# Performance work log

Measured on AMD Instinct MI355X. Metric: run time of the kernel, lower is better.

## Reference

```python
import jax, jax.numpy as jnp
import numpy as np

B, T, I, H = 64, 512, 512, 1024

def setup_inputs() -> dict:
    key = jax.random.key(0)
    ks = jax.random.split(key, 12)
    s_i = 1.0 / np.sqrt(I)
    s_h = 1.0 / np.sqrt(H)
    inp = {
        'x': jax.random.normal(ks[0], (B, T, I), dtype=jnp.float32),
        'h0': jnp.zeros((B, H), dtype=jnp.float32),
        'Wz': jax.random.uniform(ks[1], (H, I), jnp.float32, -s_i, s_i),
        'bz': jax.random.uniform(ks[2], (H,), jnp.float32, -s_i, s_i),
        'Uz': jax.random.uniform(ks[3], (H, H), jnp.float32, -s_h, s_h),
        'Wr': jax.random.uniform(ks[4], (H, I), jnp.float32, -s_i, s_i),
        'br': jax.random.uniform(ks[5], (H,), jnp.float32, -s_i, s_i),
        'Ur': jax.random.uniform(ks[6], (H, H), jnp.float32, -s_h, s_h),
        'Wh': jax.random.uniform(ks[7], (H, I), jnp.float32, -s_i, s_i),
        'bh': jax.random.uniform(ks[8], (H,), jnp.float32, -s_i, s_i),
        'Uh': jax.random.uniform(ks[9], (H, H), jnp.float32, -s_h, s_h),
    }
    return inp

def reference(x, h0, Wz, bz, Uz, Wr, br, Ur, Wh, bh, Uh):
    # Precompute all input projections for every timestep in 3 big GEMMs
    xz = jnp.einsum('bti,hi->bth', x, Wz) + bz  # [B,T,H]
    xr = jnp.einsum('bti,hi->bth', x, Wr) + br
    xh = jnp.einsum('bti,hi->bth', x, Wh) + bh
    # scan over time (recurrence)
    xs = (jnp.swapaxes(xz, 0, 1), jnp.swapaxes(xr, 0, 1), jnp.swapaxes(xh, 0, 1))  # [T,B,H]

    def step(h, inp):
        xz_t, xr_t, xh_t = inp
        z = jax.nn.sigmoid(xz_t + h @ Uz.T)
        r = jax.nn.sigmoid(xr_t + h @ Ur.T)
        h_tilde = jnp.tanh(xh_t + (r * h) @ Uh.T)
        h_new = (1.0 - z) * h + z * h_tilde
        return h_new, h_new

    h_last, outs = jax.lax.scan(step, h0, xs)  # outs: [T,B,H]
    outputs = jnp.swapaxes(outs, 0, 1)  # [B,T,H]
    return outputs, h_last
```

## Files before the change

kernel.cpp:

```cpp
#include <hip/hip_runtime.h>
#include <hip/hip_bf16.h>
#include <stdint.h>


#define B_ 64
#define T_ 512
#define I_ 512
#define H_ 1024
#define NWG_A 128
#define NWG_B 64
#define NWG 192
#define FSTR 64

typedef __attribute__((ext_vector_type(4))) float f32x4;
typedef __attribute__((ext_vector_type(8))) short s16x8;

__device__ __forceinline__ unsigned short f2bf(float f) {
  union { float f; uint32_t u; } v; v.f = f;
  uint32_t u = v.u;
  u += 0x7fffu + ((u >> 16) & 1u);
  return (unsigned short)(u >> 16);
}
__device__ __forceinline__ float bf2f(unsigned short h) {
  union { uint32_t u; float f; } v; v.u = ((uint32_t)h) << 16;
  return v.f;
}

__device__ __forceinline__ void sc_store_f32(float* p, float v) {
  asm volatile("global_store_dword %0, %1, off sc0 sc1"
               :: "v"(p), "v"(v) : "memory");
}
__device__ __forceinline__ void sc_store_u16(uint16_t* p, unsigned v) {
  asm volatile("global_store_short %0, %1, off sc0 sc1"
               :: "v"(p), "v"(v) : "memory");
}
__device__ __forceinline__ void sc_store_u32(unsigned* p, unsigned v) {
  asm volatile("global_store_dword %0, %1, off sc0 sc1"
               :: "v"(p), "v"(v) : "memory");
}
__device__ __forceinline__ s16x8 sc0_load_b128(const uint16_t* p) {
  s16x8 r;
  asm volatile("global_load_dwordx4 %0, %1, off sc0"
               : "=v"(r) : "v"(p) : "memory");
  return r;
}
__device__ __forceinline__ float sc0_load_f32(const float* p) {
  float r;
  asm volatile("global_load_dword %0, %1, off sc0"
               : "=v"(r) : "v"(p) : "memory");
  return r;
}
__device__ __forceinline__ void vm_drain() {
  asm volatile("s_waitcnt vmcnt(0)" ::: "memory");
}

__global__ void k_split(const float* __restrict__ src, uint16_t* __restrict__ dst,
                        int kshift, int total) {
  int K = 1 << kshift;
  for (int i = blockIdx.x * blockDim.x + threadIdx.x; i < total;
       i += gridDim.x * blockDim.x) {
    int n = i >> kshift, k = i & (K - 1);
    float f = src[i];
    unsigned short hi = f2bf(f);
    unsigned short lo = f2bf(f - bf2f(hi));
    size_t base = (size_t)n * (3 * K);
    dst[base + k] = hi;
    dst[base + K + k] = lo;
    dst[base + 2 * K + k] = hi;
  }
}

__global__ void k_init(const float* __restrict__ h0, float* __restrict__ h,
                       uint16_t* __restrict__ h2) {
  for (int i = blockIdx.x * blockDim.x + threadIdx.x; i < B_ * H_;
       i += gridDim.x * blockDim.x) {
    float f = h0[i];
    h[i] = f;
    int b = i >> 10, j = i & 1023;
    unsigned short hi = f2bf(f);
    h2[b * 2048 + j] = hi;
    h2[b * 2048 + 1024 + j] = f2bf(f - bf2f(hi));
  }
}

__global__ __launch_bounds__(256) void k_proj(
    const float* __restrict__ x, const uint16_t* __restrict__ W2,
    const float* __restrict__ bz, const float* __restrict__ br,
    const float* __restrict__ bh,
    float* __restrict__ XP, int t0, int Tc, int MT) {
  __shared__ uint16_t As[128][72];
  __shared__ uint16_t Bs[128][72];
  int bid = blockIdx.x;
  int mt = bid % MT, nt = bid / MT;
  int tid = threadIdx.x;
  int w = tid >> 6, l = tid & 63;
  int wm = w >> 1, wn = w & 1;
  int lr = l & 15, lg = l >> 4;

  int gr[4], gc8[4];
  const float* asrc[4];
  const uint16_t* bsrc[4];
#pragma unroll
  for (int g = 0; g < 4; ++g) {
    int gran = tid + 256 * g;
    int r = gran >> 3, c8 = gran & 7;
    gr[g] = r; gc8[g] = c8;
    int n = mt * 128 + r;
    int b = n / Tc, tt = n % Tc;
    asrc[g] = x + ((size_t)b * T_ + (t0 + tt)) * I_;
    bsrc[g] = W2 + (size_t)(nt * 128 + r) * 1536;
  }

  f32x4 acc[4][4];
#pragma unroll
  for (int mi = 0; mi < 4; ++mi)
#pragma unroll
    for (int ni = 0; ni < 4; ++ni) {
      acc[mi][ni][0] = 0.f; acc[mi][ni][1] = 0.f;
      acc[mi][ni][2] = 0.f; acc[mi][ni][3] = 0.f;
    }

  float4 pa[8];
  uint4 pb[4];
#pragma unroll
  for (int g = 0; g < 4; ++g) {
    int kp = gc8[g] * 8;
    int xc = kp & 511;
    pa[2 * g] = *(const float4*)(asrc[g] + xc);
    pa[2 * g + 1] = *(const float4*)(asrc[g] + xc + 4);
    pb[g] = *(const uint4*)(bsrc[g] + kp);
  }

  for (int it = 0; it < 24; ++it) {
    __syncthreads();
    {
      int k0 = it * 64;
#pragma unroll
      for (int g = 0; g < 4; ++g) {
        int kp = k0 + gc8[g] * 8;
        bool lofl = (kp >= 1024);
        const float* pf = (const float*)&pa[2 * g];
        s16x8 v;
#pragma unroll
        for (int j = 0; j < 8; ++j) {
          float f = pf[j];
          unsigned short hi = f2bf(f);
          v[j] = (short)(lofl ? f2bf(f - bf2f(hi)) : hi);
        }
        *(s16x8*)(&As[gr[g]][gc8[g] * 8]) = v;
        *(uint4*)(&Bs[gr[g]][gc8[g] * 8]) = pb[g];
      }
    }
    if (it + 1 < 24) {
      int k0 = (it + 1) * 64;
#pragma unroll
      for (int g = 0; g < 4; ++g) {
        int kp = k0 + gc8[g] * 8;
        int xc = kp & 511;
        pa[2 * g] = *(const float4*)(asrc[g] + xc);
        pa[2 * g + 1] = *(const float4*)(asrc[g] + xc + 4);
        pb[g] = *(const uint4*)(bsrc[g] + kp);
      }
    }
    __syncthreads();
#pragma unroll
    for (int kk = 0; kk < 64; kk += 32) {
      s16x8 af[4], bf[4];
#pragma unroll
      for (int mi = 0; mi < 4; ++mi)
        af[mi] = *(const s16x8*)(&As[wm * 64 + mi * 16 + lr][kk + lg * 8]);
#pragma unroll
      for (int ni = 0; ni < 4; ++ni)
        bf[ni] = *(const s16x8*)(&Bs[wn * 64 + ni * 16 + lr][kk + lg * 8]);
#pragma unroll
      for (int mi = 0; mi < 4; ++mi)
#pragma unroll
        for (int ni = 0; ni < 4; ++ni)
          acc[mi][ni] = __builtin_amdgcn_mfma_f32_16x16x32_bf16(
              af[mi], bf[ni], acc[mi][ni], 0, 0, 0);
    }
  }

  int g_ = (nt * 128) >> 10;
  const float* bias = (g_ == 0) ? bz : ((g_ == 1) ? br : bh);
#pragma unroll
  for (int ni = 0; ni < 4; ++ni) {
    int col = nt * 128 + wn * 64 + ni * 16 + lr;
    int jc = col & 1023;
    float bv = bias[jc];
#pragma unroll
    for (int mi = 0; mi < 4; ++mi) {
      int nrow = mt * 128 + wm * 64 + mi * 16 + lg * 4;
      int b = nrow / Tc, tt = nrow % Tc;
#pragma unroll
      for (int v = 0; v < 4; ++v) {
        XP[((size_t)((tt * 3 + g_) * 64 + b)) * 1024 + jc] = acc[mi][ni][v] + bv;
        if (++tt == Tc) { tt = 0; ++b; }
      }
    }
  }
}

__global__ __launch_bounds__(512) void k_recur(
    const float* __restrict__ Uz, const float* __restrict__ Ur,
    const float* __restrict__ Uh, const float* __restrict__ XP,
    int t0i, int Tcc, float* __restrict__ h, uint16_t* __restrict__ h2,
    uint16_t* __restrict__ s2, float* __restrict__ zbuf,
    float* __restrict__ out, unsigned* __restrict__ flagsA,
    unsigned* __restrict__ flagsB) {
  __shared__ uint16_t Wl[16 * 2048];
  __shared__ float red[8 * 64 * 17];

  const int tid = threadIdx.x;
  const int w = tid >> 6, l = tid & 63;
  const int lr = l & 15, lg = l >> 4;
  const int bid = blockIdx.x;
  const bool isA = (bid < NWG_A);
  const int tile = isA ? bid : (bid - NWG_A);
  const int n0 = tile * 16;
  const bool isR = isA && (n0 >= 1024);

  const float* src = isA ? ((n0 < 1024) ? (Uz + (size_t)n0 * 1024)
                                        : (Ur + (size_t)(n0 - 1024) * 1024))
                         : (Uh + (size_t)n0 * 1024);
  for (int i = tid; i < 2048; i += 512) {
    int r = i >> 7;
    int k8 = (i & 127) * 8;
    const float* p = src + r * 1024 + k8;
    s16x8 hi8, lo8;
#pragma unroll
    for (int j = 0; j < 8; ++j) {
      float f = p[j];
      unsigned short hb = f2bf(f);
      hi8[j] = (short)hb;
      lo8[j] = (short)f2bf(f - bf2f(hb));
    }
    uint8_t* rowp = (uint8_t*)Wl + r * 4096;
    int swz = (r & 7) << 4;
    *(s16x8*)(rowp + ((k8 * 2) ^ swz)) = hi8;
    *(s16x8*)(rowp + (((1024 + k8) * 2) ^ swz)) = lo8;
  }
  __syncthreads();

  const int KB0 = w * 128;
  const int bswz = (lr & 7) << 4;
  const uint8_t* browp = (const uint8_t*)Wl + lr * 4096;

  int eb[2], ec[2];
#pragma unroll
  for (int u = 0; u < 2; ++u) {
    int e = tid + u * 512;
    eb[u] = e >> 4; ec[u] = e & 15;
  }

  float hreg[2];
  if (!isA) {
#pragma unroll
    for (int u = 0; u < 2; ++u)
      hreg[u] = h[eb[u] * 1024 + (n0 + ec[u])];
  }

  for (int tt = 0; tt < Tcc; ++tt) {
    const unsigned t = (unsigned)(t0i + tt);

    float xpre[2];
    {
      int gate = isA ? (isR ? 1 : 0) : 2;
#pragma unroll
      for (int u = 0; u < 2; ++u) {
        int jc = (n0 + ec[u]) & 1023;
        xpre[u] = XP[((size_t)(tt * 3 + gate) * 64 + eb[u]) * 1024 + jc];
      }
    }

    if (isA) {
      if (t > 0 && w == 0) {
        const unsigned* fp = flagsB + (size_t)l * FSTR;
        for (;;) {
          unsigned f;
          asm volatile("global_load_dword %0, %1, off sc0 sc1\n\t"
                       "s_waitcnt vmcnt(0)"
                       : "=v"(f) : "v"(fp) : "memory");
          if (__all(f >= t)) break;
          __builtin_amdgcn_s_sleep(4);
        }
        if (l == 0)
          (void)__hip_atomic_load(flagsB, __ATOMIC_ACQUIRE,
                                  __HIP_MEMORY_SCOPE_AGENT);
        vm_drain();
      }
      __syncthreads();

      float hpre[2];
      if (isR) {
#pragma unroll
        for (int u = 0; u < 2; ++u)
          hpre[u] = sc0_load_f32(h + eb[u] * 1024 + (n0 - 1024 + ec[u]));
      }

      s16x8 ah[4][4], al[4][4];
#pragma unroll
      for (int ks = 0; ks < 4; ++ks)
#pragma unroll
        for (int mi = 0; mi < 4; ++mi)
          ah[ks][mi] = sc0_load_b128(h2 + (size_t)(lr + 16 * mi) * 2048 +
                                     (KB0 + ks * 32 + lg * 8));
#pragma unroll
      for (int ks = 0; ks < 4; ++ks)
#pragma unroll
        for (int mi = 0; mi < 4; ++mi)
          al[ks][mi] = sc0_load_b128(h2 + (size_t)(lr + 16 * mi) * 2048 +
                                     (1024 + KB0 + ks * 32 + lg * 8));

      f32x4 acc[4];
#pragma unroll
      for (int mi = 0; mi < 4; ++mi) {
        acc[mi][0] = 0.f; acc[mi][1] = 0.f; acc[mi][2] = 0.f; acc[mi][3] = 0.f;
      }

      asm volatile("s_waitcnt vmcnt(16)" ::: "memory");
      __builtin_amdgcn_sched_barrier(0);
      s16x8 bfv0[4];
#pragma unroll
      for (int ks = 0; ks < 4; ++ks) {
        int kp = KB0 + ks * 32 + lg * 8;
        bfv0[ks] = *(const s16x8*)(browp + ((kp * 2) ^ bswz));
#pragma unroll
        for (int mi = 0; mi < 4; ++mi)
          acc[mi] = __builtin_amdgcn_mfma_f32_16x16x32_bf16(ah[ks][mi], bfv0[ks],
                                                            acc[mi], 0, 0, 0);
      }
#pragma unroll
      for (int ks = 0; ks < 4; ++ks) {
        int kp = KB0 + ks * 32 + lg * 8;
        s16x8 bfv = *(const s16x8*)(browp + (((1024 + kp) * 2) ^ bswz));
#pragma unroll
        for (int mi = 0; mi < 4; ++mi)
          acc[mi] = __builtin_amdgcn_mfma_f32_16x16x32_bf16(ah[ks][mi], bfv,
                                                            acc[mi], 0, 0, 0);
      }
      vm_drain();
      __builtin_amdgcn_sched_barrier(0);
#pragma unroll
      for (int ks = 0; ks < 4; ++ks)
#pragma unroll
        for (int mi = 0; mi < 4; ++mi)
          acc[mi] = __builtin_amdgcn_mfma_f32_16x16x32_bf16(al[ks][mi], bfv0[ks],
                                                            acc[mi], 0, 0, 0);
#pragma unroll
      for (int mi = 0; mi < 4; ++mi)
#pragma unroll
        for (int v = 0; v < 4; ++v)
          red[(w * 64 + mi * 16 + lg * 4 + v) * 17 + lr] = acc[mi][v];
      __syncthreads();

#pragma unroll
      for (int u = 0; u < 2; ++u) {
        int b = eb[u], c = ec[u];
        float s = 0.f;
#pragma unroll
        for (int q = 0; q < 8; ++q) s += red[(q * 64 + b) * 17 + c];
        float pre = s + xpre[u];
        if (!isR) {
          int n = n0 + c;
          sc_store_f32(zbuf + b * 1024 + n, 1.f / (1.f + __expf(-pre)));
        } else {
          int j = n0 - 1024 + c;
          float r = 1.f / (1.f + __expf(-pre));
          float sv = r * hpre[u];
          unsigned short hb = f2bf(sv);
          sc_store_u16(s2 + b * 2048 + j, hb);
          sc_store_u16(s2 + b * 2048 + 1024 + j, f2bf(sv - bf2f(hb)));
        }
      }
      vm_drain();
      __syncthreads();
      if (tid == 0) sc_store_u32(flagsA + (size_t)tile * FSTR, t + 1);
    } else {
      if (w == 0) {
        const unsigned* fp0 = flagsA + (size_t)(2 * l) * FSTR;
        const unsigned* fp1 = flagsA + (size_t)(2 * l + 1) * FSTR;
        unsigned tgt = t + 1;
        for (;;) {
          unsigned f0, f1;
          asm volatile("global_load_dword %0, %2, off sc0 sc1\n\t"
                       "global_load_dword %1, %3, off sc0 sc1\n\t"
                       "s_waitcnt vmcnt(0)"
                       : "=v"(f0), "=v"(f1) : "v"(fp0), "v"(fp1) : "memory");
          if (__all((f0 >= tgt) && (f1 >= tgt))) break;
          __builtin_amdgcn_s_sleep(4);
        }
        if (l == 0)
          (void)__hip_atomic_load(flagsA, __ATOMIC_ACQUIRE,
                                  __HIP_MEMORY_SCOPE_AGENT);
        vm_drain();
      }
      __syncthreads();

      float zpre[2];
#pragma unroll
      for (int u = 0; u < 2; ++u)
        zpre[u] = sc0_load_f32(zbuf + eb[u] * 1024 + (n0 + ec[u]));

      s16x8 ah[4][4], al[4][4];
#pragma unroll
      for (int ks = 0; ks < 4; ++ks)
#pragma unroll
        for (int mi = 0; mi < 4; ++mi)
          ah[ks][mi] = sc0_load_b128(s2 + (size_t)(lr + 16 * mi) * 2048 +
                                     (KB0 + ks * 32 + lg * 8));
#pragma unroll
      for (int ks = 0; ks < 4; ++ks)
#pragma unroll
        for (int mi = 0; mi < 4; ++mi)
          al[ks][mi] = sc0_load_b128(s2 + (size_t)(lr + 16 * mi) * 2048 +
                                     (1024 + KB0 + ks * 32 + lg * 8));

      f32x4 acc[4];
#pragma unroll
      for (int mi = 0; mi < 4; ++mi) {
        acc[mi][0] = 0.f; acc[mi][1] = 0.f; acc[mi][2] = 0.f; acc[mi][3] = 0.f;
      }

      asm volatile("s_waitcnt vmcnt(16)" ::: "memory");
      __builtin_amdgcn_sched_barrier(0);
      s16x8 bfv0[4];
#pragma unroll
      for (int ks = 0; ks < 4; ++ks) {
        int kp = KB0 + ks * 32 + lg * 8;
        bfv0[ks] = *(const s16x8*)(browp + ((kp * 2) ^ bswz));
#pragma unroll
        for (int mi = 0; mi < 4; ++mi)
          acc[mi] = __builtin_amdgcn_mfma_f32_16x16x32_bf16(ah[ks][mi], bfv0[ks],
                                                            acc[mi], 0, 0, 0);
      }
#pragma unroll
      for (int ks = 0; ks < 4; ++ks) {
        int kp = KB0 + ks * 32 + lg * 8;
        s16x8 bfv = *(const s16x8*)(browp + (((1024 + kp) * 2) ^ bswz));
#pragma unroll
        for (int mi = 0; mi < 4; ++mi)
          acc[mi] = __builtin_amdgcn_mfma_f32_16x16x32_bf16(ah[ks][mi], bfv,
                                                            acc[mi], 0, 0, 0);
      }
      vm_drain();
      __builtin_amdgcn_sched_barrier(0);
#pragma unroll
      for (int ks = 0; ks < 4; ++ks)
#pragma unroll
        for (int mi = 0; mi < 4; ++mi)
          acc[mi] = __builtin_amdgcn_mfma_f32_16x16x32_bf16(al[ks][mi], bfv0[ks],
                                                            acc[mi], 0, 0, 0);
#pragma unroll
      for (int mi = 0; mi < 4; ++mi)
#pragma unroll
        for (int v = 0; v < 4; ++v)
          red[(w * 64 + mi * 16 + lg * 4 + v) * 17 + lr] = acc[mi][v];
      __syncthreads();

#pragma unroll
      for (int u = 0; u < 2; ++u) {
        int b = eb[u], c = ec[u];
        float s = 0.f;
#pragma unroll
        for (int q = 0; q < 8; ++q) s += red[(q * 64 + b) * 17 + c];
        int j = n0 + c;
        float pre = s + xpre[u];
        float ht = tanhf(pre);
        float z = zpre[u];
        float hv = hreg[u];
        float hn = (1.f - z) * hv + z * ht;
        hreg[u] = hn;
        sc_store_f32(h + b * 1024 + j, hn);
        unsigned short hb = f2bf(hn);
        sc_store_u16(h2 + b * 2048 + j, hb);
        sc_store_u16(h2 + b * 2048 + 1024 + j, f2bf(hn - bf2f(hb)));
        sc_store_f32(out + ((size_t)b * T_ + (t0i + tt)) * 1024 + j, hn);
        if (t0i + tt == T_ - 1)
          sc_store_f32(out + (size_t)B_ * T_ * 1024 + b * 1024 + j, hn);
      }
      vm_drain();
      __syncthreads();
      if (tid == 0) sc_store_u32(flagsB + (size_t)tile * FSTR, t + 1);
    }
  }
}

extern "C" void kernel_launch(void* const* d_in, const int* in_sizes, int n_in,
                              void* d_out, int out_size, void* d_ws, size_t ws_size,
                              hipStream_t stream) {
  const float* x  = (const float*)d_in[0];
  const float* h0 = (const float*)d_in[1];
  const float* Wz = (const float*)d_in[2];
  const float* bz = (const float*)d_in[3];
  const float* Uz = (const float*)d_in[4];
  const float* Wr = (const float*)d_in[5];
  const float* br = (const float*)d_in[6];
  const float* Ur = (const float*)d_in[7];
  const float* Wh = (const float*)d_in[8];
  const float* bh = (const float*)d_in[9];
  const float* Uh = (const float*)d_in[10];
  float* out = (float*)d_out;

  uint8_t* ws = (uint8_t*)d_ws;
  uint16_t* W2    = (uint16_t*)(ws + 0);
  float*    hbuf  = (float*)   (ws + 9437184);
  uint16_t* h2    = (uint16_t*)(ws + 9699328);
  uint16_t* s2    = (uint16_t*)(ws + 9961472);
  float*    zbuf  = (float*)   (ws + 10223616);
  unsigned* flagsA= (unsigned*)(ws + 10485760);
  unsigned* flagsB= (unsigned*)(ws + 10518528);
  float*    XP    = (float*)   (ws + 10534912);

  hipMemsetAsync((void*)flagsA, 0, 49152, stream);

  k_split<<<512, 256, 0, stream>>>(Wz, W2, 9, 1024 * 512);
  k_split<<<512, 256, 0, stream>>>(Wr, W2 + (size_t)1024 * 1536, 9, 1024 * 512);
  k_split<<<512, 256, 0, stream>>>(Wh, W2 + (size_t)2048 * 1536, 9, 1024 * 512);
  k_init<<<64, 256, 0, stream>>>(h0, hbuf, h2);

  size_t avail = (ws_size > 10534912u) ? (ws_size - 10534912u) : 0u;
  long long tcl = (long long)(avail / 786432u);
  int Tc = (tcl > 512) ? 512 : (int)tcl;
  Tc &= ~1;
  if (Tc < 2) Tc = 2;

  for (int t0 = 0; t0 < T_; t0 += Tc) {
    int Tcc = (Tc < T_ - t0) ? Tc : (T_ - t0);
    int MT = (B_ * Tcc) / 128;
    k_proj<<<MT * 24, 256, 0, stream>>>(x, W2, bz, br, bh, XP, t0, Tcc, MT);

    int t0v = t0, tccv = Tcc;
    void* args[] = {(void*)&Uz, (void*)&Ur, (void*)&Uh, (void*)&XP,
                    (void*)&t0v, (void*)&tccv, (void*)&hbuf, (void*)&h2,
                    (void*)&s2, (void*)&zbuf, (void*)&out,
                    (void*)&flagsA, (void*)&flagsB};
    hipLaunchCooperativeKernel((void*)k_recur, dim3(NWG), dim3(512),
                               args, 0, stream);
  }
}
```

Measured before the change: 15.89 ms.

## Vectorize recurrent-step gate stores via shared staging and drop fp32 h exchange

Gate epilogues now write per-element results to a shared sums buffer, then one thread in four computes eight consecutive columns and issues 128-bit system-coherent stores (zbuf, s2, h2) instead of many scalar 16/32-bit stores. The r-gate blocks rebuild h from the bf16 hi/lo split in h2 rather than loading the fp32 h array, so fp32 h is written only at chunk end and out uses plain stores. This cuts the number of cross-workgroup coherent memory transactions on the serial critical path. The cost is an extra barrier plus fewer active threads in the epilogue, and h reconstructed from hi+lo may differ slightly from fp32.

```diff
diff --git a/kernel.cpp b/kernel.cpp
--- a/kernel.cpp
+++ b/kernel.cpp
@@ -26,12 +26,12 @@
   return v.f;
 }
 
-__device__ __forceinline__ void sc_store_f32(float* p, float v) {
-  asm volatile("global_store_dword %0, %1, off sc0 sc1"
+__device__ __forceinline__ void sc_store_b128(uint16_t* p, s16x8 v) {
+  asm volatile("global_store_dwordx4 %0, %1, off sc0 sc1"
                :: "v"(p), "v"(v) : "memory");
 }
-__device__ __forceinline__ void sc_store_u16(uint16_t* p, unsigned v) {
-  asm volatile("global_store_short %0, %1, off sc0 sc1"
+__device__ __forceinline__ void sc_store_f32x4(float* p, f32x4 v) {
+  asm volatile("global_store_dwordx4 %0, %1, off sc0 sc1"
                :: "v"(p), "v"(v) : "memory");
 }
 __device__ __forceinline__ void sc_store_u32(unsigned* p, unsigned v) {
@@ -44,9 +44,9 @@
                : "=v"(r) : "v"(p) : "memory");
   return r;
 }
-__device__ __forceinline__ float sc0_load_f32(const float* p) {
-  float r;
-  asm volatile("global_load_dword %0, %1, off sc0"
+__device__ __forceinline__ f32x4 sc0_load_f32x4(const float* p) {
+  f32x4 r;
+  asm volatile("global_load_dwordx4 %0, %1, off sc0"
                : "=v"(r) : "v"(p) : "memory");
   return r;
 }
@@ -210,6 +210,7 @@
     unsigned* __restrict__ flagsB) {
   __shared__ uint16_t Wl[16 * 2048];
   __shared__ float red[8 * 64 * 17];
+  __shared__ float sums[64 * 17];
 
   const int tid = threadIdx.x;
   const int w = tid >> 6, l = tid & 63;
@@ -253,15 +254,19 @@
     eb[u] = e >> 4; ec[u] = e & 15;
   }
 
-  float hreg[2];
-  if (!isA) {
-#pragma unroll
-    for (int u = 0; u < 2; ++u)
-      hreg[u] = h[eb[u] * 1024 + (n0 + ec[u])];
+  const bool isStorer = ((tid & 3) == 0);
+  const int sidx = tid >> 2;
+  const int sb = sidx >> 1, sc8 = (sidx & 1) * 8;
+
+  float hreg8[8] = {0.f, 0.f, 0.f, 0.f, 0.f, 0.f, 0.f, 0.f};
+  if (!isA && isStorer) {
+    const float* hp = h + sb * 1024 + n0 + sc8;
+#pragma unroll
+    for (int q = 0; q < 8; ++q) hreg8[q] = hp[q];
   }
 
   for (int tt = 0; tt < Tcc; ++tt) {
-    const unsigned t = (unsigned)(t0i + tt);
+    const int t = t0i + tt;
 
     float xpre[2];
     {
@@ -281,7 +286,7 @@
           asm volatile("global_load_dword %0, %1, off sc0 sc1\n\t"
                        "s_waitcnt vmcnt(0)"
                        : "=v"(f) : "v"(fp) : "memory");
-          if (__all(f >= t)) break;
+          if (__all(f >= (unsigned)t)) break;
           __builtin_amdgcn_s_sleep(4);
         }
         if (l == 0)
@@ -291,13 +296,6 @@
       }
       __syncthreads();
 
-      float hpre[2];
-      if (isR) {
-#pragma unroll
-        for (int u = 0; u < 2; ++u)
-          hpre[u] = sc0_load_f32(h + eb[u] * 1024 + (n0 - 1024 + ec[u]));
-      }
-
       s16x8 ah[4][4], al[4][4];
 #pragma unroll
       for (int ks = 0; ks < 4; ++ks)
@@ -360,27 +358,49 @@
         float s = 0.f;
 #pragma unroll
         for (int q = 0; q < 8; ++q) s += red[(q * 64 + b) * 17 + c];
-        float pre = s + xpre[u];
+        sums[b * 17 + c] = s + xpre[u];
+      }
+      __syncthreads();
+
+      if (isStorer) {
         if (!isR) {
-          int n = n0 + c;
-          sc_store_f32(zbuf + b * 1024 + n, 1.f / (1.f + __expf(-pre)));
+          f32x4 z0, z1;
+#pragma unroll
+          for (int q = 0; q < 8; ++q) {
+            float pre = sums[sb * 17 + sc8 + q];
+            float zq = 1.f / (1.f + __expf(-pre));
+            if (q < 4) z0[q] = zq; else z1[q - 4] = zq;
+          }
+          sc_store_f32x4(zbuf + sb * 1024 + n0 + sc8, z0);
+          sc_store_f32x4(zbuf + sb * 1024 + n0 + sc8 + 4, z1);
         } else {
-          int j = n0 - 1024 + c;
-          float r = 1.f / (1.f + __expf(-pre));
-          float sv = r * hpre[u];
-          unsigned short hb = f2bf(sv);
-          sc_store_u16(s2 + b * 2048 + j, hb);
-          sc_store_u16(s2 + b * 2048 + 1024 + j, f2bf(sv - bf2f(hb)));
+          int j = n0 - 1024 + sc8;
+          s16x8 hh = sc0_load_b128(h2 + sb * 2048 + j);
+          s16x8 hl = sc0_load_b128(h2 + sb * 2048 + 1024 + j);
+          vm_drain();
+          s16x8 shi, slo;
+#pragma unroll
+          for (int q = 0; q < 8; ++q) {
+            float pre = sums[sb * 17 + sc8 + q];
+            float r = 1.f / (1.f + __expf(-pre));
+            float hv = bf2f((unsigned short)hh[q]) + bf2f((unsigned short)hl[q]);
+            float sv = r * hv;
+            unsigned short hb = f2bf(sv);
+            shi[q] = (short)hb;
+            slo[q] = (short)f2bf(sv - bf2f(hb));
+          }
+          sc_store_b128(s2 + sb * 2048 + j, shi);
+          sc_store_b128(s2 + sb * 2048 + 1024 + j, slo);
         }
       }
       vm_drain();
       __syncthreads();
-      if (tid == 0) sc_store_u32(flagsA + (size_t)tile * FSTR, t + 1);
+      if (tid == 0) sc_store_u32(flagsA + (size_t)tile * FSTR, (unsigned)(t + 1));
     } else {
       if (w == 0) {
         const unsigned* fp0 = flagsA + (size_t)(2 * l) * FSTR;
         const unsigned* fp1 = flagsA + (size_t)(2 * l + 1) * FSTR;
-        unsigned tgt = t + 1;
+        unsigned tgt = (unsigned)(t + 1);
         for (;;) {
           unsigned f0, f1;
           asm volatile("global_load_dword %0, %2, off sc0 sc1\n\t"
@@ -397,10 +417,11 @@
       }
       __syncthreads();
 
-      float zpre[2];
-#pragma unroll
-      for (int u = 0; u < 2; ++u)
-        zpre[u] = sc0_load_f32(zbuf + eb[u] * 1024 + (n0 + ec[u]));
+      f32x4 zp0, zp1;
+      if (isStorer) {
+        zp0 = sc0_load_f32x4(zbuf + sb * 1024 + n0 + sc8);
+        zp1 = sc0_load_f32x4(zbuf + sb * 1024 + n0 + sc8 + 4);
+      }
 
       s16x8 ah[4][4], al[4][4];
 #pragma unroll
@@ -422,7 +443,7 @@
         acc[mi][0] = 0.f; acc[mi][1] = 0.f; acc[mi][2] = 0.f; acc[mi][3] = 0.f;
       }
 
-      asm volatile("s_waitcnt vmcnt(16)" ::: "memory");
+      asm volatile("s_waitcnt vmcnt(18)" ::: "memory");
       __builtin_amdgcn_sched_barrier(0);
       s16x8 bfv0[4];
 #pragma unroll
@@ -464,24 +485,42 @@
         float s = 0.f;
 #pragma unroll
         for (int q = 0; q < 8; ++q) s += red[(q * 64 + b) * 17 + c];
-        int j = n0 + c;
-        float pre = s + xpre[u];
-        float ht = tanhf(pre);
-        float z = zpre[u];
-        float hv = hreg[u];
-        float hn = (1.f - z) * hv + z * ht;
-        hreg[u] = hn;
-        sc_store_f32(h + b * 1024 + j, hn);
-        unsigned short hb = f2bf(hn);
-        sc_store_u16(h2 + b * 2048 + j, hb);
-        sc_store_u16(h2 + b * 2048 + 1024 + j, f2bf(hn - bf2f(hb)));
-        sc_store_f32(out + ((size_t)b * T_ + (t0i + tt)) * 1024 + j, hn);
-        if (t0i + tt == T_ - 1)
-          sc_store_f32(out + (size_t)B_ * T_ * 1024 + b * 1024 + j, hn);
+        sums[b * 17 + c] = s + xpre[u];
+      }
+      __syncthreads();
+
+      if (isStorer) {
+        int j = n0 + sc8;
+        s16x8 hhi, hlo;
+        f32x4 o0, o1;
+#pragma unroll
+        for (int q = 0; q < 8; ++q) {
+          float pre = sums[sb * 17 + sc8 + q];
+          float ht = tanhf(pre);
+          float z = (q < 4) ? zp0[q] : zp1[q - 4];
+          float hn = (1.f - z) * hreg8[q] + z * ht;
+          hreg8[q] = hn;
+          unsigned short hb = f2bf(hn);
+          hhi[q] = (short)hb;
+          hlo[q] = (short)f2bf(hn - bf2f(hb));
+          if (q < 4) o0[q] = hn; else o1[q - 4] = hn;
+        }
+        sc_store_b128(h2 + sb * 2048 + j, hhi);
+        sc_store_b128(h2 + sb * 2048 + 1024 + j, hlo);
+        *(f32x4*)(out + ((size_t)sb * T_ + t) * 1024 + j) = o0;
+        *(f32x4*)(out + ((size_t)sb * T_ + t) * 1024 + j + 4) = o1;
+        if (t == T_ - 1) {
+          *(f32x4*)(out + (size_t)B_ * T_ * 1024 + sb * 1024 + j) = o0;
+          *(f32x4*)(out + (size_t)B_ * T_ * 1024 + sb * 1024 + j + 4) = o1;
+        }
+        if (tt == Tcc - 1) {
+          *(f32x4*)(h + sb * 1024 + j) = o0;
+          *(f32x4*)(h + sb * 1024 + j + 4) = o1;
+        }
       }
       vm_drain();
       __syncthreads();
-      if (tid == 0) sc_store_u32(flagsB + (size_t)tile * FSTR, t + 1);
+      if (tid == 0) sc_store_u32(flagsB + (size_t)tile * FSTR, (unsigned)(t + 1));
     }
   }
 }
```

Measured after the change: 23.79 ms. +49.7%, slower.
